# Performance work log

Measured on AMD Instinct MI355X. Metric: run time of the kernel, lower is better.

## Reference

```python
import math
import jax, jax.numpy as jnp
import numpy as np

N_HEADS = 32
N_KV_HEADS = 8
HEAD_DIM = 64
DIM = 2048
BATCH = 1
SEQ = 2048


def setup_inputs() -> dict:
    key = jax.random.key(0)
    ks = jax.random.split(key, 7)
    x = jax.random.normal(ks[0], (BATCH, SEQ, DIM), dtype=jnp.float32)
    # RoPE frequencies, llama2.c style: [seq_len, head_dim//2]
    inv_freq = 1.0 / (10000.0 ** (np.arange(0, HEAD_DIM, 2, dtype=np.float32) / HEAD_DIM))
    t = np.arange(SEQ, dtype=np.float32)
    freqs = np.outer(t, inv_freq)  # [SEQ, HEAD_DIM//2]
    freqs_cos = jnp.asarray(np.cos(freqs), dtype=jnp.float32)
    freqs_sin = jnp.asarray(np.sin(freqs), dtype=jnp.float32)
    s = 0.02
    wq = jax.random.normal(ks[1], (N_HEADS * HEAD_DIM, DIM), dtype=jnp.float32) * s
    wk = jax.random.normal(ks[2], (N_KV_HEADS * HEAD_DIM, DIM), dtype=jnp.float32) * s
    wv = jax.random.normal(ks[3], (N_KV_HEADS * HEAD_DIM, DIM), dtype=jnp.float32) * s
    wo = jax.random.normal(ks[4], (DIM, N_HEADS * HEAD_DIM), dtype=jnp.float32) * s
    return {"x": x, "freqs_cos": freqs_cos, "freqs_sin": freqs_sin,
            "wq": wq, "wk": wk, "wv": wv, "wo": wo}


def _apply_rotary(q, k, cos, sin):
    # q: [B,S,H,D], k: [B,S,Hkv,D]; cos/sin: [S, D//2]
    def rot(t):
        tr = t[..., 0::2]  # real parts (even lanes)
        ti = t[..., 1::2]  # imag parts (odd lanes)
        c = cos[None, :, None, :]
        s = sin[None, :, None, :]
        out_r = tr * c - ti * s
        out_i = tr * s + ti * c
        # re-interleave
        return jnp.stack([out_r, out_i], axis=-1).reshape(t.shape)
    return rot(q), rot(k)


def reference(x, freqs_cos, freqs_sin, wq, wk, wv, wo):
    B, S, _ = x.shape
    n_rep = N_HEADS // N_KV_HEADS
    xq = (x @ wq.T).reshape(B, S, N_HEADS, HEAD_DIM)
    xk = (x @ wk.T).reshape(B, S, N_KV_HEADS, HEAD_DIM)
    xv = (x @ wv.T).reshape(B, S, N_KV_HEADS, HEAD_DIM)
    xq, xk = _apply_rotary(xq, xk, freqs_cos, freqs_sin)
    # repeat_kv: [B,S,Hkv,D] -> [B,S,Hkv*n_rep,D]
    xk = jnp.repeat(xk, n_rep, axis=2)
    xv = jnp.repeat(xv, n_rep, axis=2)
    # [B,H,S,D]
    q = xq.transpose(0, 2, 1, 3)
    k = xk.transpose(0, 2, 1, 3)
    v = xv.transpose(0, 2, 1, 3)
    scores = jnp.einsum('bhqd,bhkd->bhqk', q, k) / math.sqrt(HEAD_DIM)
    causal = jnp.triu(jnp.ones((S, S), dtype=bool), k=1)
    scores = jnp.where(causal[None, None], -jnp.inf, scores)
    weights = jax.nn.softmax(scores, axis=-1)
    out = jnp.einsum('bhqk,bhkd->bhqd', weights, v)
    out = out.transpose(0, 2, 1, 3).reshape(B, S, N_HEADS * HEAD_DIM)
    return out @ wo.T
```

## Files before the change

### kernel.cpp

```cpp
#include <hip/hip_runtime.h>
#include <hip/hip_bf16.h>

#define DIM 2048
#define SEQ 2048
#define HD 64
#define NH 32
#define NKV 8

typedef __bf16 bf16x8 __attribute__((ext_vector_type(8)));
typedef __bf16 bf16x4 __attribute__((ext_vector_type(4)));
typedef float f32x4 __attribute__((ext_vector_type(4)));
typedef unsigned short ushortx8 __attribute__((ext_vector_type(8)));
typedef unsigned short ushortx4 __attribute__((ext_vector_type(4)));
typedef unsigned short ushort_t;

#define QSCALE 0.1803368801111f

__device__ __forceinline__ unsigned short f2bf(float f) {
    unsigned int u = __builtin_bit_cast(unsigned int, f);
    u = (u + 0x7FFFu + ((u >> 16) & 1u)) >> 16;
    return (unsigned short)u;
}

__device__ __forceinline__ f32x4 mfma16(bf16x8 a, bf16x8 b, f32x4 c) {
    return __builtin_amdgcn_mfma_f32_16x16x32_bf16(a, b, c, 0, 0, 0);
}

__device__ __forceinline__ void gload16(const ushort_t* g, ushort_t* l) {
    __builtin_amdgcn_global_load_lds(
        (const __attribute__((address_space(1))) unsigned int*)g,
        (__attribute__((address_space(3))) unsigned int*)l, 16, 0, 0);
}

#define NX  (SEQ * DIM)
#define NWQ (DIM * DIM)
#define NWK (NKV * HD * DIM)
#define NWO (DIM * NH * HD)

__global__ __launch_bounds__(256)
void cvt5(const float* __restrict__ x, const float* __restrict__ wq,
          const float* __restrict__ wk, const float* __restrict__ wv,
          const float* __restrict__ wo,
          ushort_t* __restrict__ xb, ushort_t* __restrict__ wqb,
          ushort_t* __restrict__ wkb, ushort_t* __restrict__ wvb,
          ushort_t* __restrict__ wob)
{
    const int S0 = NX / 4, S1 = S0 + NWQ / 4, S2 = S1 + NWK / 4,
              S3 = S2 + NWK / 4, S4 = S3 + NWO / 4;
    for (int g = blockIdx.x * blockDim.x + threadIdx.x; g < S4;
         g += gridDim.x * blockDim.x) {
        const float* src; ushort_t* dst; int off;
        if (g < S0)      { src = x;  dst = xb;  off = g; }
        else if (g < S1) { src = wq; dst = wqb; off = g - S0; }
        else if (g < S2) { src = wk; dst = wkb; off = g - S1; }
        else if (g < S3) { src = wv; dst = wvb; off = g - S2; }
        else             { src = wo; dst = wob; off = g - S3; }
        float4 v = ((const float4*)src)[off];
        ushortx4 h = { f2bf(v.x), f2bf(v.y), f2bf(v.z), f2bf(v.w) };
        ((ushortx4*)dst)[off] = h;
    }
}

__global__ __launch_bounds__(256)
void qkv_rope(const ushort_t* __restrict__ xb,
              const ushort_t* __restrict__ wqb, const ushort_t* __restrict__ wkb,
              const ushort_t* __restrict__ wvb,
              ushort_t* __restrict__ Qb, ushort_t* __restrict__ Kb,
              ushort_t* __restrict__ VtG,
              const float* __restrict__ cosp, const float* __restrict__ sinp)
{
    __shared__ ushort_t As[2][128 * 64];
    __shared__ ushort_t Bs[2][64 * 64];

    const int nt = blockIdx.x;
    const ushort_t* Bw; int bn0; int seg;
    if (nt < 32)      { seg = 0; Bw = wqb; bn0 = nt * 64; }
    else if (nt < 40) { seg = 1; Bw = wkb; bn0 = (nt - 32) * 64; }
    else              { seg = 2; Bw = wvb; bn0 = (nt - 40) * 64; }

    const int tid  = threadIdx.x;
    const int lane = tid & 63;
    const int wid  = tid >> 6;
    const int wr = wid >> 1, wc = wid & 1;
    const int bm0 = blockIdx.y * 128;
    const int g16 = lane >> 4, l16 = lane & 15;
    const int sr  = tid >> 3;
    const int scb = (tid & 7) * 16;
    const int scsw = (scb ^ ((sr & 7) << 4)) >> 1;
    const int xorb = (l16 & 7) << 4;

    f32x4 acc[4][2] = {};

    auto STAGE = [&](int k0, int b) {
#pragma unroll
        for (int i = 0; i < 4; i++) {
            int r = sr + i * 32;
            gload16(xb + (size_t)(bm0 + r) * DIM + k0 + scsw, &As[b][(i * 256 + tid) * 8]);
        }
#pragma unroll
        for (int i = 0; i < 2; i++) {
            int r = sr + i * 32;
            gload16(Bw + (size_t)(bn0 + r) * DIM + k0 + scsw, &Bs[b][(i * 256 + tid) * 8]);
        }
    };

    STAGE(0, 0);

    for (int k0 = 0; k0 < DIM; k0 += 64) {
        const int b = (k0 >> 6) & 1;
        __syncthreads();
        if (k0 + 64 < DIM) STAGE(k0 + 64, b ^ 1);
#pragma unroll
        for (int kk = 0; kk < 2; kk++) {
            const int ci = ((kk * 64 + g16 * 16) ^ xorb) >> 1;
            bf16x8 af[4], bfr[2];
#pragma unroll
            for (int mi = 0; mi < 4; mi++)
                af[mi] = *(const bf16x8*)&As[b][(wr * 64 + mi * 16 + l16) * 64 + ci];
#pragma unroll
            for (int ni = 0; ni < 2; ni++)
                bfr[ni] = *(const bf16x8*)&Bs[b][(wc * 32 + ni * 16 + l16) * 64 + ci];
#pragma unroll
            for (int mi = 0; mi < 4; mi++)
#pragma unroll
                for (int ni = 0; ni < 2; ni++)
                    acc[mi][ni] = mfma16(af[mi], bfr[ni], acc[mi][ni]);
        }
    }

#pragma unroll
    for (int mi = 0; mi < 4; mi++) {
#pragma unroll
        for (int ni = 0; ni < 2; ni++) {
            const int row0 = bm0 + wr * 64 + mi * 16 + g16 * 4;
            const int col  = bn0 + wc * 32 + ni * 16 + l16;
            f32x4 v = acc[mi][ni];
            if (seg <= 1) {
                ushort_t* C = (seg == 0) ? Qb : Kb;
                const int ldC = (seg == 0) ? NH * HD : NKV * HD;
                const int d   = col & (HD - 1);
                const int p   = d >> 1;
                const bool odd = d & 1;
#pragma unroll
                for (int r = 0; r < 4; r++) {
                    float val = v[r];
                    float partner = __shfl_xor(val, 1);
                    int m = row0 + r;
                    float c = cosp[m * (HD / 2) + p];
                    float s = sinp[m * (HD / 2) + p];
                    float o = odd ? (partner * s + val * c) : (val * c - partner * s);
                    if (seg == 0) o *= QSCALE;
                    C[(size_t)m * ldC + col] = f2bf(o);
                }
            } else {
                ushortx4 hv = { f2bf(v[0]), f2bf(v[1]), f2bf(v[2]), f2bf(v[3]) };
                *(ushortx4*)&VtG[(size_t)col * SEQ + row0] = hv;
            }
        }
    }
}

__global__ __launch_bounds__(256)
void attn_fwd(const ushort_t* __restrict__ Q,
              const ushort_t* __restrict__ K,
              const ushort_t* __restrict__ VtG,
              ushort_t* __restrict__ O)
{
    __shared__ ushort_t Ks[2][64 * 64];
    __shared__ ushort_t Vt[2][64 * 64];
    __shared__ ushort_t Ps[4 * 16 * 72];

    const int h  = blockIdx.x;
    const int qi = 31 - blockIdx.y;
    const int kh = h >> 2;
    const int tid = threadIdx.x;
    const int lane = tid & 63;
    const int w = tid >> 6;
    const int g16 = lane >> 4, l16 = lane & 15;
    const int sr = tid >> 3;
    const int scb = (tid & 7) * 16;
    const int scsw = (scb ^ ((sr & 7) << 4)) >> 1;
    const int xorb = (l16 & 7) << 4;

    const int qw = qi * 64 + w * 16;
    const int nkt = qi + 1;

    bf16x8 qf[2];
#pragma unroll
    for (int kk = 0; kk < 2; kk++)
        qf[kk] = *(const bf16x8*)&Q[(size_t)(qw + l16) * (NH * HD) + h * HD + kk * 32 + g16 * 8];

    f32x4 oacc[4] = {};
    float lsum = 0.f;

    auto STAGE = [&](int kt, int bf) {
#pragma unroll
        for (int i = 0; i < 2; i++) {
            int row = sr + i * 32;
            gload16(K   + (size_t)(kt * 64 + row) * (NKV * HD) + kh * HD + scsw,
                    &Ks[bf][(i * 256 + tid) * 8]);
            gload16(VtG + (size_t)(kh * HD + row) * SEQ + kt * 64 + scsw,
                    &Vt[bf][(i * 256 + tid) * 8]);
        }
    };

    STAGE(0, 0);

    for (int kj = 0; kj < nkt; kj++) {
        const int b = kj & 1;
        const int kb = kj * 64;
        __syncthreads();
        if (kj + 1 < nkt) STAGE(kj + 1, b ^ 1);

        f32x4 sacc[4] = {};
        __builtin_amdgcn_s_setprio(1);
#pragma unroll
        for (int kk = 0; kk < 2; kk++) {
            const int ci = ((kk * 64 + g16 * 16) ^ xorb) >> 1;
#pragma unroll
            for (int nf = 0; nf < 4; nf++) {
                bf16x8 kf = *(const bf16x8*)&Ks[b][(nf * 16 + l16) * 64 + ci];
                sacc[nf] = mfma16(kf, qf[kk], sacc[nf]);
            }
        }
        __builtin_amdgcn_s_setprio(0);
        const int qg = qw + l16;
        if (kb + 63 > qw) {
#pragma unroll
            for (int nf = 0; nf < 4; nf++) {
#pragma unroll
                for (int r = 0; r < 4; r++) {
                    int kg = kb + nf * 16 + g16 * 4 + r;
                    if (kg > qg) sacc[nf][r] = -1e30f;
                }
            }
        }
#pragma unroll
        for (int nf = 0; nf < 4; nf++) {
            float p0 = exp2f(sacc[nf][0]);
            float p1 = exp2f(sacc[nf][1]);
            float p2 = exp2f(sacc[nf][2]);
            float p3 = exp2f(sacc[nf][3]);
            lsum += (p0 + p1) + (p2 + p3);
            bf16x4 pk = { (__bf16)p0, (__bf16)p1, (__bf16)p2, (__bf16)p3 };
            *(bf16x4*)&Ps[(w * 16 + l16) * 72 + nf * 16 + g16 * 4] = pk;
        }
        asm volatile("s_waitcnt lgkmcnt(0)" ::: "memory");
        __builtin_amdgcn_s_setprio(1);
#pragma unroll
        for (int kk = 0; kk < 2; kk++) {
            const int ci = ((kk * 64 + g16 * 16) ^ xorb) >> 1;
            bf16x8 pf = *(const bf16x8*)&Ps[(w * 16 + l16) * 72 + kk * 32 + g16 * 8];
#pragma unroll
            for (int df = 0; df < 4; df++) {
                bf16x8 vf = *(const bf16x8*)&Vt[b][(df * 16 + l16) * 64 + ci];
                oacc[df] = mfma16(pf, vf, oacc[df]);
            }
        }
        __builtin_amdgcn_s_setprio(0);
    }

    lsum += __shfl_xor(lsum, 16);
    lsum += __shfl_xor(lsum, 32);
#pragma unroll
    for (int r = 0; r < 4; r++) {
        float ls = __shfl(lsum, g16 * 16 + g16 * 4 + r);
        float inv = 1.0f / ls;
#pragma unroll
        for (int df = 0; df < 4; df++)
            O[(size_t)(qw + g16 * 4 + r) * (NH * HD) + h * HD + df * 16 + l16] =
                f2bf(oacc[df][r] * inv);
    }
}

__global__ __launch_bounds__(256)
void gemm_out(const ushort_t* __restrict__ A, const ushort_t* __restrict__ Bw,
              float* __restrict__ C)
{
    __shared__ ushort_t As[2][128 * 64];
    __shared__ ushort_t Bs[2][64 * 64];

    const int tid  = threadIdx.x;
    const int lane = tid & 63;
    const int wid  = tid >> 6;
    const int wr = wid >> 1, wc = wid & 1;
    const int bm0 = blockIdx.y * 128, bn0 = blockIdx.x * 64;
    const int g16 = lane >> 4, l16 = lane & 15;
    const int sr  = tid >> 3;
    const int scb = (tid & 7) * 16;
    const int scsw = (scb ^ ((sr & 7) << 4)) >> 1;
    const int xorb = (l16 & 7) << 4;

    f32x4 acc[4][2] = {};

    auto STAGE = [&](int k0, int b) {
#pragma unroll
        for (int i = 0; i < 4; i++) {
            int r = sr + i * 32;
            gload16(A + (size_t)(bm0 + r) * DIM + k0 + scsw, &As[b][(i * 256 + tid) * 8]);
        }
#pragma unroll
        for (int i = 0; i < 2; i++) {
            int r = sr + i * 32;
            gload16(Bw + (size_t)(bn0 + r) * DIM + k0 + scsw, &Bs[b][(i * 256 + tid) * 8]);
        }
    };

    STAGE(0, 0);

    for (int k0 = 0; k0 < DIM; k0 += 64) {
        const int b = (k0 >> 6) & 1;
        __syncthreads();
        if (k0 + 64 < DIM) STAGE(k0 + 64, b ^ 1);
#pragma unroll
        for (int kk = 0; kk < 2; kk++) {
            const int ci = ((kk * 64 + g16 * 16) ^ xorb) >> 1;
            bf16x8 af[4], bfr[2];
#pragma unroll
            for (int mi = 0; mi < 4; mi++)
                af[mi] = *(const bf16x8*)&As[b][(wr * 64 + mi * 16 + l16) * 64 + ci];
#pragma unroll
            for (int ni = 0; ni < 2; ni++)
                bfr[ni] = *(const bf16x8*)&Bs[b][(wc * 32 + ni * 16 + l16) * 64 + ci];
#pragma unroll
            for (int mi = 0; mi < 4; mi++)
#pragma unroll
                for (int ni = 0; ni < 2; ni++)
                    acc[mi][ni] = mfma16(af[mi], bfr[ni], acc[mi][ni]);
        }
    }

#pragma unroll
    for (int mi = 0; mi < 4; mi++) {
#pragma unroll
        for (int ni = 0; ni < 2; ni++) {
            const int row0 = bm0 + wr * 64 + mi * 16 + g16 * 4;
            const int col  = bn0 + wc * 32 + ni * 16 + l16;
#pragma unroll
            for (int r = 0; r < 4; r++)
                C[(size_t)(row0 + r) * DIM + col] = acc[mi][ni][r];
        }
    }
}

extern "C" void kernel_launch(void* const* d_in, const int* in_sizes, int n_in,
                              void* d_out, int out_size, void* d_ws, size_t ws_size,
                              hipStream_t stream)
{
    (void)in_sizes; (void)n_in; (void)out_size; (void)ws_size;
    const float* x    = (const float*)d_in[0];
    const float* fcos = (const float*)d_in[1];
    const float* fsin = (const float*)d_in[2];
    const float* wq   = (const float*)d_in[3];
    const float* wk   = (const float*)d_in[4];
    const float* wv   = (const float*)d_in[5];
    const float* wo   = (const float*)d_in[6];
    float* out = (float*)d_out;

    char* ws = (char*)d_ws;
    size_t off = 0;
    ushort_t* xb  = (ushort_t*)(ws + off); off += (size_t)NX  * 2;
    ushort_t* wqb = (ushort_t*)(ws + off); off += (size_t)NWQ * 2;
    ushort_t* wkb = (ushort_t*)(ws + off); off += (size_t)NWK * 2;
    ushort_t* wvb = (ushort_t*)(ws + off); off += (size_t)NWK * 2;
    ushort_t* wob = (ushort_t*)(ws + off); off += (size_t)NWO * 2;
    ushort_t* Qb  = (ushort_t*)(ws + off); off += (size_t)SEQ * NH * HD * 2;
    ushort_t* Kb  = (ushort_t*)(ws + off); off += (size_t)SEQ * NKV * HD * 2;
    ushort_t* VtG = (ushort_t*)(ws + off); off += (size_t)SEQ * NKV * HD * 2;
    ushort_t* Ab  = (ushort_t*)(ws + off);

    dim3 blk(256);
    cvt5<<<dim3(2048), blk, 0, stream>>>(x, wq, wk, wv, wo, xb, wqb, wkb, wvb, wob);
    qkv_rope<<<dim3(48, 16), blk, 0, stream>>>(xb, wqb, wkb, wvb, Qb, Kb, VtG, fcos, fsin);
    attn_fwd<<<dim3(32, 32), blk, 0, stream>>>(Qb, Kb, VtG, Ab);
    gemm_out<<<dim3(32, 16), blk, 0, stream>>>(Ab, wob, out);
}
```

Baseline: 124.5 us.

## Switch attention to 32x32x16 MFMA with 128-row Q tiles and register-resident P

```diff
diff --git a/kernel.cpp b/kernel.cpp
--- a/kernel.cpp
+++ b/kernel.cpp
@@ -10,6 +10,7 @@
 typedef __bf16 bf16x8 __attribute__((ext_vector_type(8)));
 typedef __bf16 bf16x4 __attribute__((ext_vector_type(4)));
 typedef float f32x4 __attribute__((ext_vector_type(4)));
+typedef float f32x16 __attribute__((ext_vector_type(16)));
 typedef unsigned short ushortx8 __attribute__((ext_vector_type(8)));
 typedef unsigned short ushortx4 __attribute__((ext_vector_type(4)));
 typedef unsigned short ushort_t;
@@ -24,6 +25,9 @@
 
 __device__ __forceinline__ f32x4 mfma16(bf16x8 a, bf16x8 b, f32x4 c) {
     return __builtin_amdgcn_mfma_f32_16x16x32_bf16(a, b, c, 0, 0, 0);
+}
+__device__ __forceinline__ f32x16 mfma32(bf16x8 a, bf16x8 b, f32x16 c) {
+    return __builtin_amdgcn_mfma_f32_32x32x16_bf16(a, b, c, 0, 0, 0);
 }
 
 __device__ __forceinline__ void gload16(const ushort_t* g, ushort_t* l) {
@@ -153,8 +157,10 @@
                     C[(size_t)m * ldC + col] = f2bf(o);
                 }
             } else {
+                const int pg = ((g16 & 1) << 1) | (g16 >> 1);
+                const int rowp = bm0 + wr * 64 + mi * 16 + pg * 4;
                 ushortx4 hv = { f2bf(v[0]), f2bf(v[1]), f2bf(v[2]), f2bf(v[3]) };
-                *(ushortx4*)&VtG[(size_t)col * SEQ + row0] = hv;
+                *(ushortx4*)&VtG[(size_t)col * SEQ + rowp] = hv;
             }
         }
     }
@@ -168,29 +174,29 @@
 {
     __shared__ ushort_t Ks[2][64 * 64];
     __shared__ ushort_t Vt[2][64 * 64];
-    __shared__ ushort_t Ps[4 * 16 * 72];
 
     const int h  = blockIdx.x;
-    const int qi = 31 - blockIdx.y;
+    const int qi = 15 - blockIdx.y;
     const int kh = h >> 2;
     const int tid = threadIdx.x;
     const int lane = tid & 63;
     const int w = tid >> 6;
-    const int g16 = lane >> 4, l16 = lane & 15;
+    const int l32 = lane & 31;
+    const int hi  = lane >> 5;
     const int sr = tid >> 3;
     const int scb = (tid & 7) * 16;
     const int scsw = (scb ^ ((sr & 7) << 4)) >> 1;
-    const int xorb = (l16 & 7) << 4;
-
-    const int qw = qi * 64 + w * 16;
-    const int nkt = qi + 1;
-
-    bf16x8 qf[2];
-#pragma unroll
-    for (int kk = 0; kk < 2; kk++)
-        qf[kk] = *(const bf16x8*)&Q[(size_t)(qw + l16) * (NH * HD) + h * HD + kk * 32 + g16 * 8];
-
-    f32x4 oacc[4] = {};
+    const int rxor = (l32 & 7) << 4;
+
+    const int qw = qi * 128 + w * 32;
+    const int nkt = 2 * qi + 2;
+
+    bf16x8 qf[4];
+#pragma unroll
+    for (int ds = 0; ds < 4; ds++)
+        qf[ds] = *(const bf16x8*)&Q[(size_t)(qw + l32) * (NH * HD) + h * HD + ds * 16 + hi * 8];
+
+    f32x16 accO0 = {}, accO1 = {};
     float lsum = 0.f;
 
     auto STAGE = [&](int kt, int bf) {
@@ -212,64 +218,65 @@
         __syncthreads();
         if (kj + 1 < nkt) STAGE(kj + 1, b ^ 1);
 
-        f32x4 sacc[4] = {};
-        __builtin_amdgcn_s_setprio(1);
-#pragma unroll
-        for (int kk = 0; kk < 2; kk++) {
-            const int ci = ((kk * 64 + g16 * 16) ^ xorb) >> 1;
-#pragma unroll
-            for (int nf = 0; nf < 4; nf++) {
-                bf16x8 kf = *(const bf16x8*)&Ks[b][(nf * 16 + l16) * 64 + ci];
-                sacc[nf] = mfma16(kf, qf[kk], sacc[nf]);
-            }
-        }
-        __builtin_amdgcn_s_setprio(0);
-        const int qg = qw + l16;
-        if (kb + 63 > qw) {
-#pragma unroll
-            for (int nf = 0; nf < 4; nf++) {
-#pragma unroll
-                for (int r = 0; r < 4; r++) {
-                    int kg = kb + nf * 16 + g16 * 4 + r;
-                    if (kg > qg) sacc[nf][r] = -1e30f;
+        if (kb <= qw + 31) {
+            f32x16 s0 = {}, s1 = {};
+            __builtin_amdgcn_s_setprio(1);
+#pragma unroll
+            for (int ds = 0; ds < 4; ds++) {
+                const int cb = (32 * ds + 16 * hi);
+                bf16x8 kf0 = *(const bf16x8*)&Ks[b][(l32)      * 64 + ((cb ^ ((l32 & 7) << 4)) >> 1)];
+                bf16x8 kf1 = *(const bf16x8*)&Ks[b][(32 + l32) * 64 + ((cb ^ ((l32 & 7) << 4)) >> 1)];
+                s0 = mfma32(kf0, qf[ds], s0);
+                s1 = mfma32(kf1, qf[ds], s1);
+            }
+            __builtin_amdgcn_s_setprio(0);
+
+            if (kb + 63 > qw) {
+                const int qg = qw + l32;
+#pragma unroll
+                for (int r = 0; r < 16; r++) {
+                    const int kl = (r & 3) + 8 * (r >> 2) + 4 * hi;
+                    if (kb + kl > qg)      s0[r] = -1e30f;
+                    if (kb + 32 + kl > qg) s1[r] = -1e30f;
                 }
             }
-        }
-#pragma unroll
-        for (int nf = 0; nf < 4; nf++) {
-            float p0 = exp2f(sacc[nf][0]);
-            float p1 = exp2f(sacc[nf][1]);
-            float p2 = exp2f(sacc[nf][2]);
-            float p3 = exp2f(sacc[nf][3]);
-            lsum += (p0 + p1) + (p2 + p3);
-            bf16x4 pk = { (__bf16)p0, (__bf16)p1, (__bf16)p2, (__bf16)p3 };
-            *(bf16x4*)&Ps[(w * 16 + l16) * 72 + nf * 16 + g16 * 4] = pk;
-        }
-        asm volatile("s_waitcnt lgkmcnt(0)" ::: "memory");
-        __builtin_amdgcn_s_setprio(1);
-#pragma unroll
-        for (int kk = 0; kk < 2; kk++) {
-            const int ci = ((kk * 64 + g16 * 16) ^ xorb) >> 1;
-            bf16x8 pf = *(const bf16x8*)&Ps[(w * 16 + l16) * 72 + kk * 32 + g16 * 8];
-#pragma unroll
-            for (int df = 0; df < 4; df++) {
-                bf16x8 vf = *(const bf16x8*)&Vt[b][(df * 16 + l16) * 64 + ci];
-                oacc[df] = mfma16(pf, vf, oacc[df]);
-            }
-        }
-        __builtin_amdgcn_s_setprio(0);
-    }
-
-    lsum += __shfl_xor(lsum, 16);
+
+            float p0[16], p1[16];
+#pragma unroll
+            for (int r = 0; r < 16; r++) { p0[r] = exp2f(s0[r]); p1[r] = exp2f(s1[r]); }
+#pragma unroll
+            for (int r = 0; r < 16; r++) lsum += p0[r] + p1[r];
+            bf16x8 pa00, pa01, pa10, pa11;
+#pragma unroll
+            for (int e = 0; e < 8; e++) {
+                pa00[e] = (__bf16)p0[e];  pa01[e] = (__bf16)p0[8 + e];
+                pa10[e] = (__bf16)p1[e];  pa11[e] = (__bf16)p1[8 + e];
+            }
+
+            __builtin_amdgcn_s_setprio(1);
+#pragma unroll
+            for (int s = 0; s < 4; s++) {
+                bf16x8 pa = (s == 0) ? pa00 : (s == 1) ? pa01 : (s == 2) ? pa10 : pa11;
+                const int cb = (32 * s + 16 * hi);
+                bf16x8 vf0 = *(const bf16x8*)&Vt[b][(l32)      * 64 + ((cb ^ ((l32 & 7) << 4)) >> 1)];
+                bf16x8 vf1 = *(const bf16x8*)&Vt[b][(32 + l32) * 64 + ((cb ^ ((l32 & 7) << 4)) >> 1)];
+                accO0 = mfma32(pa, vf0, accO0);
+                accO1 = mfma32(pa, vf1, accO1);
+            }
+            __builtin_amdgcn_s_setprio(0);
+        }
+    }
+
     lsum += __shfl_xor(lsum, 32);
-#pragma unroll
-    for (int r = 0; r < 4; r++) {
-        float ls = __shfl(lsum, g16 * 16 + g16 * 4 + r);
+
+#pragma unroll
+    for (int r = 0; r < 16; r++) {
+        const int qr = (r & 3) + 8 * (r >> 2) + 4 * hi;
+        float ls = __shfl(lsum, qr);
         float inv = 1.0f / ls;
-#pragma unroll
-        for (int df = 0; df < 4; df++)
-            O[(size_t)(qw + g16 * 4 + r) * (NH * HD) + h * HD + df * 16 + l16] =
-                f2bf(oacc[df][r] * inv);
+        size_t base = (size_t)(qw + qr) * (NH * HD) + h * HD;
+        O[base + l32]      = f2bf(accO0[r] * inv);
+        O[base + 32 + l32] = f2bf(accO1[r] * inv);
     }
 }
 
@@ -372,6 +379,6 @@
     dim3 blk(256);
     cvt5<<<dim3(2048), blk, 0, stream>>>(x, wq, wk, wv, wo, xb, wqb, wkb, wvb, wob);
     qkv_rope<<<dim3(48, 16), blk, 0, stream>>>(xb, wqb, wkb, wvb, Qb, Kb, VtG, fcos, fsin);
-    attn_fwd<<<dim3(32, 32), blk, 0, stream>>>(Qb, Kb, VtG, Ab);
+    attn_fwd<<<dim3(32, 16), blk, 0, stream>>>(Qb, Kb, VtG, Ab);
     gemm_out<<<dim3(32, 16), blk, 0, stream>>>(Ab, wob, out);
 }
```

Measured after the change: 139.5 us. 1.12x slower.
